# Performance work log

Hardware: AMD Instinct MI355X
Metric: run time of the kernel (lower is better)

## Reference

```python
import jax, jax.numpy as jnp
import numpy as np

V, E, H, NL, B, T, LK = 50000, 512, 256, 3, 32, 512, 148  # vocab, embed, hidden, total bi-GRU layers, batch, seqlen, leak feats
EPS = 1e-3  # Keras BatchNormalization default epsilon


def setup_inputs() -> dict:
    key = jax.random.key(0)
    ks = jax.random.split(key, 24)
    s = 0.05
    inp = {
        "comment_indices": jax.random.randint(ks[0], (B, T), 0, V),
        "comment_masks": jnp.ones((B, T), jnp.float32),
        "code_indices": jax.random.randint(ks[1], (B, T), 0, V),
        "code_masks": jnp.ones((B, T), jnp.float32),
        "leaks_indices": jax.random.normal(ks[2], (B, LK), jnp.float32),
        "leaks_masks": jnp.ones((B, LK), jnp.float32),
        # parameters (all GRU layers share input dim E = 2*H by construction)
        "embed_table": jax.random.normal(ks[3], (V, E), jnp.float32) * (H ** -0.5),
        "gru_Wx": jax.random.normal(ks[4], (NL, 2, E, 3 * H), jnp.float32) * s,
        "gru_Wh": jax.random.normal(ks[5], (NL, 2, H, 3 * H), jnp.float32) * s,
        "gru_b": jax.random.normal(ks[6], (NL, 2, 2, 3 * H), jnp.float32) * s,  # [input_bias, recurrent_bias]
        "leaks_W": jax.random.normal(ks[7], (LK, 256), jnp.float32) * s,
        "leaks_b": jnp.zeros((256,), jnp.float32),
        "bn1_gamma": 1.0 + 0.1 * jax.random.normal(ks[8], (2 * H + 2 * H + 256,), jnp.float32),
        "bn1_beta": 0.1 * jax.random.normal(ks[9], (2 * H + 2 * H + 256,), jnp.float32),
        "bn1_mean": 0.1 * jax.random.normal(ks[10], (2 * H + 2 * H + 256,), jnp.float32),
        "bn1_var": jax.random.uniform(ks[11], (2 * H + 2 * H + 256,), jnp.float32, 0.5, 1.5),
        "fc1_W": jax.random.normal(ks[12], (2 * H + 2 * H + 256, 256), jnp.float32) * s,
        "fc1_b": jnp.zeros((256,), jnp.float32),
        "bn2_gamma": 1.0 + 0.1 * jax.random.normal(ks[13], (256,), jnp.float32),
        "bn2_beta": 0.1 * jax.random.normal(ks[14], (256,), jnp.float32),
        "bn2_mean": 0.1 * jax.random.normal(ks[15], (256,), jnp.float32),
        "bn2_var": jax.random.uniform(ks[16], (256,), jnp.float32, 0.5, 1.5),
        "cls_W": jax.random.normal(ks[17], (256, 1), jnp.float32) * s,
        "cls_b": jnp.zeros((1,), jnp.float32),
    }
    return inp


def _gru(x, Wx, Wh, b):
    # Keras GRU v2: reset_after=True, gate order [z, r, h], dual bias.
    # x: [B, T, D] -> outputs [B, T, H]
    xp = jnp.einsum('btd,dg->btg', x, Wx) + b[0]  # precompute input projections

    def step(h, xt):
        rec = h @ Wh + b[1]  # [B, 3H]
        xz, xr, xh = jnp.split(xt, 3, axis=-1)
        rz, rr, rh = jnp.split(rec, 3, axis=-1)
        z = jax.nn.sigmoid(xz + rz)
        r = jax.nn.sigmoid(xr + rr)
        hh = jnp.tanh(xh + r * rh)
        h = z * h + (1.0 - z) * hh
        return h, h

    h0 = jnp.zeros((x.shape[0], Wh.shape[0]), x.dtype)
    _, ys = jax.lax.scan(step, h0, jnp.swapaxes(xp, 0, 1))  # scan over time
    return jnp.swapaxes(ys, 0, 1)


def _bigru_seq(x, Wx, Wh, b):
    f = _gru(x, Wx[0], Wh[0], b[0])
    bw = _gru(x[:, ::-1], Wx[1], Wh[1], b[1])[:, ::-1]
    return jnp.concatenate([f, bw], axis=-1)


def _bigru_last(x, Wx, Wh, b):
    f = _gru(x, Wx[0], Wh[0], b[0])[:, -1]
    bw = _gru(x[:, ::-1], Wx[1], Wh[1], b[1])[:, -1]
    return jnp.concatenate([f, bw], axis=-1)


def _encode(x, Wx, Wh, b):
    for i in range(NL - 1):
        x = _bigru_seq(x, Wx[i], Wh[i], b[i])
    return _bigru_last(x, Wx[-1], Wh[-1], b[-1])


def _bn(x, g, bt, m, v):
    return (x - m) * jax.lax.rsqrt(v + EPS) * g + bt


def reference(comment_indices, comment_masks, code_indices, code_masks, leaks_indices, leaks_masks,
              embed_table, gru_Wx, gru_Wh, gru_b, leaks_W, leaks_b,
              bn1_gamma, bn1_beta, bn1_mean, bn1_var, fc1_W, fc1_b,
              bn2_gamma, bn2_beta, bn2_mean, bn2_var, cls_W, cls_b):
    comment_em = embed_table[comment_indices]  # [B, T, E]
    code_em = embed_table[code_indices]
    code_states = _encode(code_em, gru_Wx, gru_Wh, gru_b)      # [B, 2H]
    comment_states = _encode(comment_em, gru_Wx, gru_Wh, gru_b)  # [B, 2H]
    leaks_states = jax.nn.relu(leaks_indices @ leaks_W + leaks_b)  # [B, 256]
    states = jnp.concatenate([code_states, comment_states, leaks_states], axis=-1)
    states = _bn(states, bn1_gamma, bn1_beta, bn1_mean, bn1_var)
    states = jax.nn.relu(states @ fc1_W + fc1_b)
    states = _bn(states, bn2_gamma, bn2_beta, bn2_mean, bn2_var)
    preds = jax.nn.sigmoid(states @ cls_W + cls_b)
    return jnp.squeeze(preds, -1)  # [B]
```

## Files before the change

kernel.cpp:

```cpp
#include <hip/hip_runtime.h>
#include <hip/hip_fp16.h>
#include <math.h>

typedef _Float16 f16;
typedef _Float16 f16x2 __attribute__((ext_vector_type(2)));
typedef _Float16 f16x4 __attribute__((ext_vector_type(4)));
typedef _Float16 f16x8 __attribute__((ext_vector_type(8)));
typedef float f32x2 __attribute__((ext_vector_type(2)));
typedef float f32x4 __attribute__((ext_vector_type(4)));
typedef unsigned int u32;
typedef unsigned long long u64;

#define NLAYER 3
#define BB 64
#define TT 512
#define HH 256
#define GG 768
#define EE 512
#define ROWS (BB*TT)

__device__ __forceinline__ void load_lds16(const void* g, void* l) {
  __builtin_amdgcn_global_load_lds((const __attribute__((address_space(1))) u32*)g,
                                   (__attribute__((address_space(3))) u32*)l, 16, 0, 0);
}

__device__ __forceinline__ f32x2 pk_fma(f32x2 a, f32x2 b, f32x2 c) {
  f32x2 d;
  asm("v_pk_fma_f32 %0, %1, %2, %3" : "=v"(d) : "v"(a), "v"(b), "v"(c));
  return d;
}

__device__ __forceinline__ void publish(u64* p, u32 tag, float v) {
  u64 e = ((u64)tag << 32) | (u64)__builtin_bit_cast(u32, v);
  __hip_atomic_store(p, e, __ATOMIC_RELAXED, __HIP_MEMORY_SCOPE_AGENT);
}
__device__ __forceinline__ float wait_peer(const u64* p, u32 tag) {
  u64 e;
  for (;;) {
    e = __hip_atomic_load(p, __ATOMIC_RELAXED, __HIP_MEMORY_SCOPE_AGENT);
    if ((u32)(e >> 32) == tag) break;
    __builtin_amdgcn_s_sleep(2);
  }
  return __builtin_bit_cast(float, (u32)e);
}

__global__ __launch_bounds__(256) void prep_wx(
    const float* __restrict__ Wx, f16* __restrict__ Bth, f16* __restrict__ Btl)
{
  const int n_bt = NLAYER * 2 * GG * EE;
  const int stride = gridDim.x * blockDim.x;
  for (int e = blockIdx.x * blockDim.x + threadIdx.x; e < n_bt; e += stride) {
    int l = e / (2 * GG * EE); int r = e % (2 * GG * EE);
    int n = r / EE; int k = r % EE;
    int dr = n / GG; int j = n % GG;
    float w = Wx[(((size_t)(l * 2 + dr) * EE + k) * GG) + j];
    f16 hi = (f16)w;
    Bth[e] = hi;
    Btl[e] = (f16)(w - (float)hi);
  }
}

__global__ __launch_bounds__(128) void gather_embed(
    const int* __restrict__ code_idx, const int* __restrict__ comment_idx,
    const float* __restrict__ table, f16* __restrict__ Xh, f16* __restrict__ Xl)
{
  const int r = blockIdx.x;
  const int idx = (r < 16384) ? code_idx[r] : comment_idx[r - 16384];
  const float4 v = ((const float4*)(table + (size_t)idx * EE))[threadIdx.x];
  f16x4 hi, lo;
  hi.x = (f16)v.x; lo.x = (f16)(v.x - (float)hi.x);
  hi.y = (f16)v.y; lo.y = (f16)(v.y - (float)hi.y);
  hi.z = (f16)v.z; lo.z = (f16)(v.z - (float)hi.z);
  hi.w = (f16)v.w; lo.w = (f16)(v.w - (float)hi.w);
  *(f16x4*)(Xh + (size_t)r * EE + threadIdx.x * 4) = hi;
  *(f16x4*)(Xl + (size_t)r * EE + threadIdx.x * 4) = lo;
}

__global__ __launch_bounds__(256) void gemm_split(
    const f16* __restrict__ Ah, const f16* __restrict__ Al,
    const f16* __restrict__ Bh, const f16* __restrict__ Bl,
    float* __restrict__ C)
{
  __shared__ __align__(16) f16 sAh[128 * 64];
  __shared__ __align__(16) f16 sAl[128 * 64];
  __shared__ __align__(16) f16 sBh[128 * 64];
  __shared__ __align__(16) f16 sBl[128 * 64];
  const int wg = blockIdx.x;
  const int nt = wg % 12;
  const int mt = wg / 12;
  const int t = threadIdx.x;
  const int lane = t & 63, wid = t >> 6;
  const int wr = wid >> 1, wc = wid & 1;

  f32x4 acc[4][4] = {};

  for (int ks_ = 0; ks_ < EE / 64; ++ks_) {
    const int k0 = ks_ * 64;
    if (ks_) __syncthreads();
    #pragma unroll
    for (int c = 0; c < 4; ++c) {
      const int s = c * 256 + t;
      const int row = s >> 3;
      const int g = (s & 7) ^ (row & 7);
      const size_t offA = (size_t)(mt * 128 + row) * EE + k0 + g * 8;
      const size_t offB = (size_t)(nt * 128 + row) * EE + k0 + g * 8;
      load_lds16(Ah + offA, sAh + s * 8);
      load_lds16(Al + offA, sAl + s * 8);
      load_lds16(Bh + offB, sBh + s * 8);
      load_lds16(Bl + offB, sBl + s * 8);
    }
    asm volatile("s_waitcnt vmcnt(0)" ::: "memory");
    __syncthreads();

    #pragma unroll
    for (int kk = 0; kk < 2; ++kk) {
      f16x8 ah[4], al[4], bh[4], bl[4];
      #pragma unroll
      for (int m = 0; m < 4; ++m) {
        const int r = wr * 64 + m * 16 + (lane & 15);
        const int gr = (kk * 4 + (lane >> 4)) ^ (r & 7);
        ah[m] = *(const f16x8*)((const char*)sAh + r * 128 + gr * 16);
        al[m] = *(const f16x8*)((const char*)sAl + r * 128 + gr * 16);
        const int cb = wc * 64 + m * 16 + (lane & 15);
        const int gb = (kk * 4 + (lane >> 4)) ^ (cb & 7);
        bh[m] = *(const f16x8*)((const char*)sBh + cb * 128 + gb * 16);
        bl[m] = *(const f16x8*)((const char*)sBl + cb * 128 + gb * 16);
      }
      #pragma unroll
      for (int m = 0; m < 4; ++m)
        #pragma unroll
        for (int n = 0; n < 4; ++n) {
          acc[m][n] = __builtin_amdgcn_mfma_f32_16x16x32_f16(ah[m], bh[n], acc[m][n], 0, 0, 0);
          acc[m][n] = __builtin_amdgcn_mfma_f32_16x16x32_f16(al[m], bh[n], acc[m][n], 0, 0, 0);
          acc[m][n] = __builtin_amdgcn_mfma_f32_16x16x32_f16(ah[m], bl[n], acc[m][n], 0, 0, 0);
        }
    }
  }

  const int crow0 = mt * 128 + wr * 64 + (lane >> 4) * 4;
  const int ccol0 = nt * 128 + wc * 64 + (lane & 15);
  #pragma unroll
  for (int m = 0; m < 4; ++m)
    #pragma unroll
    for (int n = 0; n < 4; ++n)
      #pragma unroll
      for (int q = 0; q < 4; ++q)
        C[(size_t)(crow0 + m * 16 + q) * (2 * GG) + ccol0 + n * 16] = acc[m][n][q];
}

__global__ __launch_bounds__(512, 2) void gru_pair(
    const float* __restrict__ xp,
    const float* __restrict__ Wh,
    const float* __restrict__ bias,
    f16* __restrict__ Xh, f16* __restrict__ Xl,
    float* __restrict__ states,
    u64* __restrict__ xchg,
    int last, int layer)
{
  const int w = blockIdx.x;
  const int job = w & 127;
  const int kh  = w >> 7;
  const int dir = job >> 6, b = job & 63;
  const int t = threadIdx.x;
  const int sub = t >> 8, jj = t & 255;

  __shared__ __align__(16) float hsm[128];
  __shared__ float part[2][GG];
  __shared__ float prez[128], prer[128], xh_s[128], rh_s[128];

  f32x2 w0[32], w1[32], w2[32];
  {
    const float* wb = Wh + (size_t)dir * (HH * GG) + (size_t)(kh * 128 + sub * 64) * GG;
    #pragma unroll
    for (int m = 0; m < 32; ++m) {
      w0[m] = f32x2{wb[(2 * m) * GG + jj      ], wb[(2 * m + 1) * GG + jj      ]};
      w1[m] = f32x2{wb[(2 * m) * GG + jj + 256], wb[(2 * m + 1) * GG + jj + 256]};
      w2[m] = f32x2{wb[(2 * m) * GG + jj + 512], wb[(2 * m + 1) * GG + jj + 512]};
    }
  }

  const int g = t >> 7, jjg = t & 127;
  const int colm = g * 256 + kh * 128 + jjg;
  const int colp = g * 256 + (1 - kh) * 128 + jjg;
  float b0c = 0.f, b1c = 0.f, xcur = 0.f;
  const float* xpb = xp + (size_t)b * TT * (2 * GG) + dir * GG;
  if (t < 384) {
    b0c = bias[dir * 2 * GG + colm];
    b1c = bias[dir * 2 * GG + GG + colm];
    xcur = xpb[(size_t)(dir ? TT - 1 : 0) * (2 * GG) + colm];
  }
  u64* pub = xchg + (size_t)(job * 2 + kh) * 2 * 384;
  const u64* peer = xchg + (size_t)(job * 2 + (1 - kh)) * 2 * 384;

  float hreg = 0.f;
  if (t < 128) hsm[t] = 0.f;
  __syncthreads();

  for (int st = 0; st < TT; ++st) {
    const int tt = dir ? (TT - 1 - st) : st;
    const u32 tag = (u32)(layer * TT + st + 1);
    const int par = st & 1;

    f32x2 a0 = {0.f, 0.f}, a1 = {0.f, 0.f}, a2 = {0.f, 0.f};
    const float4* hp = (const float4*)hsm + sub * 16;
    #pragma unroll
    for (int m = 0; m < 16; ++m) {
      const float4 q = hp[m];
      const f32x2 qa = {q.x, q.y}, qb = {q.z, q.w};
      a0 = pk_fma(qa, w0[2 * m], a0); a0 = pk_fma(qb, w0[2 * m + 1], a0);
      a1 = pk_fma(qa, w1[2 * m], a1); a1 = pk_fma(qb, w1[2 * m + 1], a1);
      a2 = pk_fma(qa, w2[2 * m], a2); a2 = pk_fma(qb, w2[2 * m + 1], a2);
    }
    part[sub][jj]       = a0.x + a0.y;
    part[sub][jj + 256] = a1.x + a1.y;
    part[sub][jj + 512] = a2.x + a2.y;
    __syncthreads();

    if (t < 384) {
      publish(pub + par * 384 + t, tag, part[0][colp] + part[1][colp]);
      float xnext = 0.f;
      if (st + 1 < TT) xnext = xpb[(size_t)(dir ? tt - 1 : tt + 1) * (2 * GG) + colm];
      const float mine = part[0][colm] + part[1][colm];
      const float pv = wait_peer(peer + par * 384 + t, tag);
      const float rec = mine + pv + b1c;
      const float xpre = xcur + b0c;
      if (g == 0)      prez[jjg] = xpre + rec;
      else if (g == 1) prer[jjg] = xpre + rec;
      else           { xh_s[jjg] = xpre; rh_s[jjg] = rec; }
      xcur = xnext;
    }
    __syncthreads();

    if (t < 128) {
      const float z = 1.f / (1.f + expf(-prez[t]));
      const float r = 1.f / (1.f + expf(-prer[t]));
      const float hh = tanhf(xh_s[t] + r * rh_s[t]);
      hreg = z * hreg + (1.f - z) * hh;
      hsm[t] = hreg;
      const int j = kh * 128 + t;
      if (!last) {
        const f16 hi = (f16)hreg;
        const size_t o = (size_t)(b * TT + tt) * EE + dir * HH + j;
        Xh[o] = hi;
        Xl[o] = (f16)(hreg - (float)hi);
      } else if (st == TT - 1) {
        states[(size_t)b * (2 * HH) + dir * HH + j] = hreg;
      }
    }
    __syncthreads();
  }
}

__global__ __launch_bounds__(256) void final_head(
    const float* __restrict__ states, const float* __restrict__ leaks_in,
    const float* __restrict__ leaks_W, const float* __restrict__ leaks_b,
    const float* __restrict__ bn1g, const float* __restrict__ bn1b,
    const float* __restrict__ bn1m, const float* __restrict__ bn1v,
    const float* __restrict__ fc1W, const float* __restrict__ fc1b,
    const float* __restrict__ bn2g, const float* __restrict__ bn2b,
    const float* __restrict__ bn2m, const float* __restrict__ bn2v,
    const float* __restrict__ clsW, const float* __restrict__ clsb,
    float* __restrict__ out)
{
  const int b = blockIdx.x;
  const int c = threadIdx.x;
  __shared__ float vec[1280];
  __shared__ float red[256];

  float acc = leaks_b[c];
  for (int k = 0; k < 148; ++k) acc += leaks_in[b * 148 + k] * leaks_W[k * 256 + c];
  vec[1024 + c] = fmaxf(acc, 0.f);
  for (int i = c; i < 512; i += 256) {
    vec[i] = states[(size_t)b * 512 + i];
    vec[512 + i] = states[(size_t)(b + 32) * 512 + i];
  }
  __syncthreads();
  for (int i = c; i < 1280; i += 256)
    vec[i] = (vec[i] - bn1m[i]) * rsqrtf(bn1v[i] + 1e-3f) * bn1g[i] + bn1b[i];
  __syncthreads();
  float a1 = fc1b[c];
  for (int i = 0; i < 1280; ++i) a1 += vec[i] * fc1W[i * 256 + c];
  a1 = fmaxf(a1, 0.f);
  a1 = (a1 - bn2m[c]) * rsqrtf(bn2v[c] + 1e-3f) * bn2g[c] + bn2b[c];
  red[c] = a1 * clsW[c];
  __syncthreads();
  for (int s = 128; s > 0; s >>= 1) { if (c < s) red[c] += red[c + s]; __syncthreads(); }
  if (c == 0) out[b] = 1.f / (1.f + expf(-(red[0] + clsb[0])));
}

extern "C" void kernel_launch(void* const* d_in, const int* in_sizes, int n_in,
                              void* d_out, int out_size, void* d_ws, size_t ws_size,
                              hipStream_t stream) {
  const int*   comment_idx = (const int*)d_in[0];
  const int*   code_idx    = (const int*)d_in[2];
  const float* leaks_in    = (const float*)d_in[4];
  const float* table       = (const float*)d_in[6];
  const float* Wx          = (const float*)d_in[7];
  const float* Wh          = (const float*)d_in[8];
  const float* gb          = (const float*)d_in[9];
  const float* leaks_W     = (const float*)d_in[10];
  const float* leaks_b     = (const float*)d_in[11];
  const float* bn1g = (const float*)d_in[12];
  const float* bn1b = (const float*)d_in[13];
  const float* bn1m = (const float*)d_in[14];
  const float* bn1v = (const float*)d_in[15];
  const float* fc1W = (const float*)d_in[16];
  const float* fc1b = (const float*)d_in[17];
  const float* bn2g = (const float*)d_in[18];
  const float* bn2b = (const float*)d_in[19];
  const float* bn2m = (const float*)d_in[20];
  const float* bn2v = (const float*)d_in[21];
  const float* clsW = (const float*)d_in[22];
  const float* clsb = (const float*)d_in[23];
  float* out = (float*)d_out;

  char* ws = (char*)d_ws;
  f16*   Xh     = (f16*)(ws);
  f16*   Xl     = (f16*)(ws + 33554432);
  float* xp     = (float*)(ws + 67108864);
  f16*   Bth    = (f16*)(ws + 268435456);
  f16*   Btl    = (f16*)(ws + 273154048);
  float* states = (float*)(ws + 277872640);
  u64*   xchg   = (u64*)(ws + 278003712);

  prep_wx<<<dim3(1024), dim3(256), 0, stream>>>(Wx, Bth, Btl);
  gather_embed<<<dim3(ROWS), dim3(128), 0, stream>>>(code_idx, comment_idx, table, Xh, Xl);

  const int gemm_grid = (ROWS / 128) * (2 * GG / 128);
  const size_t btl_stride = (size_t)2 * GG * EE;
  const size_t wh_stride  = (size_t)2 * HH * GG;

  for (int l = 0; l < NLAYER; ++l) {
    gemm_split<<<dim3(gemm_grid), dim3(256), 0, stream>>>(
        Xh, Xl, Bth + l * btl_stride, Btl + l * btl_stride, xp);
    gru_pair<<<dim3(256), dim3(512), 0, stream>>>(
        xp, Wh + l * wh_stride, gb + l * 2 * 2 * GG,
        Xh, Xl, states, xchg, l == NLAYER - 1, l);
  }

  final_head<<<dim3(32), dim3(256), 0, stream>>>(states, leaks_in, leaks_W, leaks_b,
                                                 bn1g, bn1b, bn1m, bn1v, fc1W, fc1b,
                                                 bn2g, bn2b, bn2m, bn2v, clsW, clsb, out);
}
```

Measured before the change: 3.499 ms.

## Split GRU recurrence by output columns and exchange hidden halves between block pairs

The recurrent GRU kernel is restructured so each of the two paired blocks owns 128 hidden units across all three gates (768 threads, one gate column each). Blocks now publish only their 128 new hidden values instead of 384 partial gate sums. The local half of the matvec runs while the peer's half is awaited, which overlaps the cross-block exchange with compute. Fast exp-based sigmoid and tanh replace expf and tanhf, and the spin sleep is shortened, at some cost in numerical accuracy and in register pressure from 768-thread blocks.

New measurement: 11.91 ms. 240% more time.

```diff
diff --git a/kernel.cpp b/kernel.cpp
--- a/kernel.cpp
+++ b/kernel.cpp
@@ -24,12 +24,6 @@
                                    (__attribute__((address_space(3))) u32*)l, 16, 0, 0);
 }
 
-__device__ __forceinline__ f32x2 pk_fma(f32x2 a, f32x2 b, f32x2 c) {
-  f32x2 d;
-  asm("v_pk_fma_f32 %0, %1, %2, %3" : "=v"(d) : "v"(a), "v"(b), "v"(c));
-  return d;
-}
-
 __device__ __forceinline__ void publish(u64* p, u32 tag, float v) {
   u64 e = ((u64)tag << 32) | (u64)__builtin_bit_cast(u32, v);
   __hip_atomic_store(p, e, __ATOMIC_RELAXED, __HIP_MEMORY_SCOPE_AGENT);
@@ -39,10 +33,13 @@
   for (;;) {
     e = __hip_atomic_load(p, __ATOMIC_RELAXED, __HIP_MEMORY_SCOPE_AGENT);
     if ((u32)(e >> 32) == tag) break;
-    __builtin_amdgcn_s_sleep(2);
+    __builtin_amdgcn_s_sleep(1);
   }
   return __builtin_bit_cast(float, (u32)e);
 }
+
+__device__ __forceinline__ float sigm_fast(float x) { return 1.f / (1.f + __expf(-x)); }
+__device__ __forceinline__ float tanh_fast(float x) { return 1.f - 2.f / (__expf(2.f * x) + 1.f); }
 
 __global__ __launch_bounds__(256) void prep_wx(
     const float* __restrict__ Wx, f16* __restrict__ Bth, f16* __restrict__ Btl)
@@ -148,7 +145,7 @@
         C[(size_t)(crow0 + m * 16 + q) * (2 * GG) + ccol0 + n * 16] = acc[m][n][q];
 }
 
-__global__ __launch_bounds__(512, 2) void gru_pair(
+__global__ __launch_bounds__(768, 3) void gru_cols(
     const float* __restrict__ xp,
     const float* __restrict__ Wh,
     const float* __restrict__ bias,
@@ -162,89 +159,98 @@
   const int kh  = w >> 7;
   const int dir = job >> 6, b = job & 63;
   const int t = threadIdx.x;
-  const int sub = t >> 8, jj = t & 255;
-
-  __shared__ __align__(16) float hsm[128];
-  __shared__ float part[2][GG];
-  __shared__ float prez[128], prer[128], xh_s[128], rh_s[128];
-
-  f32x2 w0[32], w1[32], w2[32];
+  const int q = t >= 384;
+  const int c = q ? t - 384 : t;
+  const int g = c >> 7, jj = c & 127;
+  const int gc = g * 256 + kh * 128 + jj;
+
+  __shared__ __align__(16) float hsm[2 * 128];
+  __shared__ float part[2][384];
+
+  const int kloc = kh * 128 + q * 64;
+  const int krem = (1 - kh) * 128 + q * 64;
+  f32x2 wl[32], wr_[32];
   {
-    const float* wb = Wh + (size_t)dir * (HH * GG) + (size_t)(kh * 128 + sub * 64) * GG;
+    const float* wb = Wh + (size_t)dir * (HH * GG) + gc;
     #pragma unroll
     for (int m = 0; m < 32; ++m) {
-      w0[m] = f32x2{wb[(2 * m) * GG + jj      ], wb[(2 * m + 1) * GG + jj      ]};
-      w1[m] = f32x2{wb[(2 * m) * GG + jj + 256], wb[(2 * m + 1) * GG + jj + 256]};
-      w2[m] = f32x2{wb[(2 * m) * GG + jj + 512], wb[(2 * m + 1) * GG + jj + 512]};
-    }
-  }
-
-  const int g = t >> 7, jjg = t & 127;
-  const int colm = g * 256 + kh * 128 + jjg;
-  const int colp = g * 256 + (1 - kh) * 128 + jjg;
-  float b0c = 0.f, b1c = 0.f, xcur = 0.f;
-  const float* xpb = xp + (size_t)b * TT * (2 * GG) + dir * GG;
-  if (t < 384) {
-    b0c = bias[dir * 2 * GG + colm];
-    b1c = bias[dir * 2 * GG + GG + colm];
-    xcur = xpb[(size_t)(dir ? TT - 1 : 0) * (2 * GG) + colm];
-  }
-  u64* pub = xchg + (size_t)(job * 2 + kh) * 2 * 384;
-  const u64* peer = xchg + (size_t)(job * 2 + (1 - kh)) * 2 * 384;
+      wl[m]  = f32x2{wb[(size_t)(kloc + 2 * m) * GG], wb[(size_t)(kloc + 2 * m + 1) * GG]};
+      wr_[m] = f32x2{wb[(size_t)(krem + 2 * m) * GG], wb[(size_t)(krem + 2 * m + 1) * GG]};
+    }
+  }
+
+  float b0z = 0.f, b0r = 0.f, b0h = 0.f, b1z = 0.f, b1r = 0.f, b1h = 0.f;
+  if (t < 128) {
+    const int cz = kh * 128 + t, cr = 256 + cz, ch = 512 + cz;
+    b0z = bias[dir * 2 * GG + cz]; b1z = bias[dir * 2 * GG + GG + cz];
+    b0r = bias[dir * 2 * GG + cr]; b1r = bias[dir * 2 * GG + GG + cr];
+    b0h = bias[dir * 2 * GG + ch]; b1h = bias[dir * 2 * GG + GG + ch];
+  }
+  const float* xpb = xp + (size_t)b * TT * (2 * GG) + dir * GG + kh * 128;
+
+  u64* pub = xchg + (size_t)(job * 2 + kh) * 256;
+  const u64* peer = xchg + (size_t)(job * 2 + (1 - kh)) * 256;
 
   float hreg = 0.f;
-  if (t < 128) hsm[t] = 0.f;
+  if (t < 256) hsm[t] = 0.f;
   __syncthreads();
 
   for (int st = 0; st < TT; ++st) {
     const int tt = dir ? (TT - 1 - st) : st;
-    const u32 tag = (u32)(layer * TT + st + 1);
-    const int par = st & 1;
-
-    f32x2 a0 = {0.f, 0.f}, a1 = {0.f, 0.f}, a2 = {0.f, 0.f};
-    const float4* hp = (const float4*)hsm + sub * 16;
-    #pragma unroll
-    for (int m = 0; m < 16; ++m) {
-      const float4 q = hp[m];
-      const f32x2 qa = {q.x, q.y}, qb = {q.z, q.w};
-      a0 = pk_fma(qa, w0[2 * m], a0); a0 = pk_fma(qb, w0[2 * m + 1], a0);
-      a1 = pk_fma(qa, w1[2 * m], a1); a1 = pk_fma(qb, w1[2 * m + 1], a1);
-      a2 = pk_fma(qa, w2[2 * m], a2); a2 = pk_fma(qb, w2[2 * m + 1], a2);
-    }
-    part[sub][jj]       = a0.x + a0.y;
-    part[sub][jj + 256] = a1.x + a1.y;
-    part[sub][jj + 512] = a2.x + a2.y;
+
+    float xz = 0.f, xr = 0.f, xh = 0.f;
+    if (t < 128) {
+      const float* xrow = xpb + (size_t)tt * (2 * GG) + t;
+      xz = xrow[0]; xr = xrow[256]; xh = xrow[512];
+    }
+    f32x2 a = {0.f, 0.f};
+    {
+      const float4* hp = (const float4*)(hsm + kloc);
+      #pragma unroll
+      for (int m = 0; m < 16; ++m) {
+        const float4 h4 = hp[m];
+        a = f32x2{h4.x, h4.y} * wl[2 * m] + a;
+        a = f32x2{h4.z, h4.w} * wl[2 * m + 1] + a;
+      }
+    }
+    if (st > 0 && t >= 640) {
+      const int pj = t - 640;
+      const float pv = wait_peer(peer + ((st + 1) & 1) * 128 + pj,
+                                 ((u32)layer << 16) | (u32)st);
+      hsm[(1 - kh) * 128 + pj] = pv;
+    }
     __syncthreads();
 
-    if (t < 384) {
-      publish(pub + par * 384 + t, tag, part[0][colp] + part[1][colp]);
-      float xnext = 0.f;
-      if (st + 1 < TT) xnext = xpb[(size_t)(dir ? tt - 1 : tt + 1) * (2 * GG) + colm];
-      const float mine = part[0][colm] + part[1][colm];
-      const float pv = wait_peer(peer + par * 384 + t, tag);
-      const float rec = mine + pv + b1c;
-      const float xpre = xcur + b0c;
-      if (g == 0)      prez[jjg] = xpre + rec;
-      else if (g == 1) prer[jjg] = xpre + rec;
-      else           { xh_s[jjg] = xpre; rh_s[jjg] = rec; }
-      xcur = xnext;
-    }
+    {
+      const float4* hp = (const float4*)(hsm + krem);
+      #pragma unroll
+      for (int m = 0; m < 16; ++m) {
+        const float4 h4 = hp[m];
+        a = f32x2{h4.x, h4.y} * wr_[2 * m] + a;
+        a = f32x2{h4.z, h4.w} * wr_[2 * m + 1] + a;
+      }
+    }
+    part[q][c] = a.x + a.y;
     __syncthreads();
 
     if (t < 128) {
-      const float z = 1.f / (1.f + expf(-prez[t]));
-      const float r = 1.f / (1.f + expf(-prer[t]));
-      const float hh = tanhf(xh_s[t] + r * rh_s[t]);
+      const float rz = part[0][t]       + part[1][t]       + b1z;
+      const float rr = part[0][128 + t] + part[1][128 + t] + b1r;
+      const float rh = part[0][256 + t] + part[1][256 + t] + b1h;
+      const float z = sigm_fast(xz + b0z + rz);
+      const float r = sigm_fast(xr + b0r + rr);
+      const float hh = tanh_fast(xh + b0h + r * rh);
       hreg = z * hreg + (1.f - z) * hh;
-      hsm[t] = hreg;
-      const int j = kh * 128 + t;
+      hsm[kh * 128 + t] = hreg;
+      if (st + 1 < TT)
+        publish(pub + (st & 1) * 128 + t, ((u32)layer << 16) | (u32)(st + 1), hreg);
       if (!last) {
         const f16 hi = (f16)hreg;
-        const size_t o = (size_t)(b * TT + tt) * EE + dir * HH + j;
+        const size_t o = (size_t)(b * TT + tt) * EE + dir * HH + kh * 128 + t;
         Xh[o] = hi;
         Xl[o] = (f16)(hreg - (float)hi);
       } else if (st == TT - 1) {
-        states[(size_t)b * (2 * HH) + dir * HH + j] = hreg;
+        states[(size_t)b * (2 * HH) + dir * HH + kh * 128 + t] = hreg;
       }
     }
     __syncthreads();
@@ -333,7 +339,7 @@
   for (int l = 0; l < NLAYER; ++l) {
     gemm_split<<<dim3(gemm_grid), dim3(256), 0, stream>>>(
         Xh, Xl, Bth + l * btl_stride, Btl + l * btl_stride, xp);
-    gru_pair<<<dim3(256), dim3(512), 0, stream>>>(
+    gru_cols<<<dim3(256), dim3(768), 0, stream>>>(
         xp, Wh + l * wh_stride, gb + l * 2 * 2 * GG,
         Xh, Xl, states, xchg, l == NLAYER - 1, l);
   }
```
